# Optimization experiments

Hardware: AMD Instinct MI355X
Metric: run time of the kernel (lower is better)

Reference implementation:

```python
import jax, jax.numpy as jnp
import numpy as np

H = 64  # hidden size

def setup_inputs() -> dict:
    key = jax.random.key(0)
    ks = jax.random.split(key, 7)
    B, T = 256, 5000
    s = 1.0 / np.sqrt(H)  # PyTorch LSTM init scale
    return {
        "x":    jax.random.normal(ks[0], (B, T), dtype=jnp.float32),
        "W_ih": jax.random.uniform(ks[1], (4 * H, 1), jnp.float32, -s, s),
        "W_hh": jax.random.uniform(ks[2], (4 * H, H), jnp.float32, -s, s),
        "b_ih": jax.random.uniform(ks[3], (4 * H,), jnp.float32, -s, s),
        "b_hh": jax.random.uniform(ks[4], (4 * H,), jnp.float32, -s, s),
        "W_fc": jax.random.uniform(ks[5], (128, H), jnp.float32, -s, s),
        "b_fc": jax.random.uniform(ks[6], (128,), jnp.float32, -s, s),
    }

def _lstm_last_hidden(x, W_ih, W_hh, b_ih, b_hh):
    # x: [B, T]; returns last hidden state h_T: [B, H]
    B, T = x.shape
    # input projection for all timesteps at once: [B, T, 4H]
    # (input_size == 1, so this is an outer product with W_ih[:, 0])
    x_proj = x[:, :, None] * W_ih[:, 0][None, None, :] + (b_ih + b_hh)

    def step(carry, xp_t):
        h, c = carry
        gates = xp_t + h @ W_hh.T  # [B, 4H]
        i = jax.nn.sigmoid(gates[:, 0 * H:1 * H])
        f = jax.nn.sigmoid(gates[:, 1 * H:2 * H])
        g = jnp.tanh(gates[:, 2 * H:3 * H])
        o = jax.nn.sigmoid(gates[:, 3 * H:4 * H])
        c = f * c + i * g
        h = o * jnp.tanh(c)
        return (h, c), None

    h0 = jnp.zeros((B, H), x.dtype)
    c0 = jnp.zeros((B, H), x.dtype)
    (h, c), _ = jax.lax.scan(step, (h0, c0), jnp.swapaxes(x_proj, 0, 1))
    return h

def reference(x, W_ih, W_hh, b_ih, b_hh, W_fc, b_fc):
    h_last = _lstm_last_hidden(x, W_ih, W_hh, b_ih, b_hh)  # [B, H]
    return jax.nn.relu(h_last @ W_fc.T + b_fc)  # [B, 128]
```

## Files before the change

kernel.cpp:

```cpp
#include <hip/hip_runtime.h>


#define LSTM_H 64
#define LSTM_T 5000
#define LSTM_B 256

typedef float v2f __attribute__((ext_vector_type(2)));

__device__ __forceinline__ void pk_fma_acc(v2f& acc, v2f a, v2f b) {
    asm("v_pk_fma_f32 %0, %1, %2, %0" : "+v"(acc) : "v"(a), "v"(b));
}

__device__ __forceinline__ float fast_rcp(float v) {
    return __builtin_amdgcn_rcpf(v);
}

__global__ __launch_bounds__(256) void ECGLSTM_lstm_fused(
    const float* __restrict__ x,
    const float* __restrict__ W_ih,
    const float* __restrict__ W_hh,
    const float* __restrict__ b_ih,
    const float* __restrict__ b_hh,
    const float* __restrict__ W_fc,
    const float* __restrict__ b_fc,
    float* __restrict__ out)
{
    const int tid  = threadIdx.x;
    const int lane = tid & 63;
    const int b    = blockIdx.x;

    __shared__ float xch[LSTM_T];
    __shared__ float hbuf[2][LSTM_H];
    __shared__ float gbuf[2][4 * LSTM_H];

    const float* xb = x + b * LSTM_T;
    for (int i = tid; i < LSTM_T; i += 256) xch[i] = xb[i];

    v2f w[LSTM_H / 2];
    {
        const float4* wrow = reinterpret_cast<const float4*>(W_hh + tid * LSTM_H);
        #pragma unroll
        for (int i = 0; i < LSTM_H / 4; ++i) {
            float4 v = wrow[i];
            w[2 * i]     = v2f{v.x, v.y};
            w[2 * i + 1] = v2f{v.z, v.w};
        }
    }
    const float wih  = W_ih[tid];
    const float bias = b_ih[tid] + b_hh[tid];
    const bool  is_tanh = ((tid >> 6) == 2);

    float c = 0.0f;
    hbuf[0][lane] = 0.0f;
    __syncthreads();

    #define LSTM_STEP(t, P)                                                    \
    {                                                                          \
        const float xv = xch[(t)];                          \
        v2f A = {0.f, 0.f}, C = {0.f, 0.f};                                    \
        const float4* h4 = reinterpret_cast<const float4*>(hbuf[(P)]);         \
        _Pragma("unroll")                                                      \
        for (int i = 0; i < LSTM_H / 4; ++i) {                                 \
            float4 hv = h4[i];                             \
            pk_fma_acc(A, v2f{hv.x, hv.y}, w[2 * i]);                          \
            pk_fma_acc(C, v2f{hv.z, hv.w}, w[2 * i + 1]);                      \
        }                                                                      \
        float g = fmaf(xv, wih, bias) + ((A.x + A.y) + (C.x + C.y));           \
        float act;                                                             \
        if (is_tanh) {                                                         \
            float e = __expf(2.0f * g);                                        \
            act = 1.0f - 2.0f * fast_rcp(e + 1.0f);                            \
        } else {                                                               \
            float e = __expf(-g);                                              \
            act = fast_rcp(1.0f + e);                                          \
        }                                                                      \
        gbuf[(P)][tid] = act;                                                  \
        __syncthreads();                                  \
        const float ig = gbuf[(P)][lane];                                      \
        const float fg = gbuf[(P)][LSTM_H + lane];                             \
        const float gg = gbuf[(P)][2 * LSTM_H + lane];                         \
        const float og = gbuf[(P)][3 * LSTM_H + lane];                         \
        c = fmaf(fg, c, ig * gg);                                              \
        float e2 = __expf(2.0f * c);                                           \
        float th = 1.0f - 2.0f * fast_rcp(e2 + 1.0f);                          \
        hbuf[1 - (P)][lane] = og * th;                    \
    }

    for (int t = 0; t < LSTM_T; t += 2) {
        LSTM_STEP(t, 0);
        LSTM_STEP(t + 1, 1);
    }
    #undef LSTM_STEP

    if (tid < 128) {
        float s = b_fc[tid];
        const float4* wf = reinterpret_cast<const float4*>(W_fc + tid * LSTM_H);
        const float4* h4 = reinterpret_cast<const float4*>(hbuf[0]);
        #pragma unroll
        for (int i = 0; i < LSTM_H / 4; ++i) {
            float4 wv = wf[i];
            float4 hv = h4[i];
            s = fmaf(hv.x, wv.x, s);
            s = fmaf(hv.y, wv.y, s);
            s = fmaf(hv.z, wv.z, s);
            s = fmaf(hv.w, wv.w, s);
        }
        out[b * 128 + tid] = fmaxf(s, 0.0f);
    }
}

extern "C" void kernel_launch(void* const* d_in, const int* in_sizes, int n_in,
                              void* d_out, int out_size, void* d_ws, size_t ws_size,
                              hipStream_t stream) {
    const float* x    = (const float*)d_in[0];
    const float* W_ih = (const float*)d_in[1];
    const float* W_hh = (const float*)d_in[2];
    const float* b_ih = (const float*)d_in[3];
    const float* b_hh = (const float*)d_in[4];
    const float* W_fc = (const float*)d_in[5];
    const float* b_fc = (const float*)d_in[6];
    float* out = (float*)d_out;

    ECGLSTM_lstm_fused<<<LSTM_B, 256, 0, stream>>>(
        x, W_ih, W_hh, b_ih, b_hh, W_fc, b_fc, out);
}
```

Before: 2.075 ms.

## Restructure LSTM step to two waves with DPP/swizzle hidden-state broadcast

Each block now runs two wavefronts instead of four, and each thread computes two gate rows. The recurrent hidden vector no longer goes through shared memory. It is broadcast inside the wave with DPP row rotates, ds_swizzle and ds_bpermute, and the weight columns are pre-permuted to match that rotated order. Only the gate activations are still exchanged between the two waves through shared memory, which cuts barrier participants and LDS traffic on the serial critical path. In exchange each thread holds twice as many weight registers and does twice the FMAs per step, and the lane-rotation permutation logic is intricate.

```diff
diff --git a/kernel.cpp b/kernel.cpp
--- a/kernel.cpp
+++ b/kernel.cpp
@@ -10,12 +10,28 @@
 __device__ __forceinline__ void pk_fma_acc(v2f& acc, v2f a, v2f b) {
     asm("v_pk_fma_f32 %0, %1, %2, %0" : "+v"(acc) : "v"(a), "v"(b));
 }
-
 __device__ __forceinline__ float fast_rcp(float v) {
     return __builtin_amdgcn_rcpf(v);
 }
+template<int J>
+__device__ __forceinline__ float row_ror(float v) {
+    if constexpr (J == 0) return v;
+    else return __builtin_bit_cast(float,
+        __builtin_amdgcn_mov_dpp(__builtin_bit_cast(int, v),
+                                 0x120 + J, 0xF, 0xF, false));
+}
+__device__ __forceinline__ float swz16(float v) {
+    return __builtin_bit_cast(float,
+        __builtin_amdgcn_ds_swizzle(__builtin_bit_cast(int, v), 0x401F));
+}
+__device__ __forceinline__ float bperm(int addr, float v) {
+    return __builtin_bit_cast(float,
+        __builtin_amdgcn_ds_bpermute(addr, __builtin_bit_cast(int, v)));
+}
 
-__global__ __launch_bounds__(256) void ECGLSTM_lstm_fused(
+__global__ __attribute__((amdgpu_flat_work_group_size(128, 128),
+                          amdgpu_waves_per_eu(1, 1)))
+void ECGLSTM_lstm_2w(
     const float* __restrict__ x,
     const float* __restrict__ W_ih,
     const float* __restrict__ W_hh,
@@ -27,63 +43,89 @@
 {
     const int tid  = threadIdx.x;
     const int lane = tid & 63;
+    const bool w1  = (tid >> 6) != 0;
     const int b    = blockIdx.x;
 
     __shared__ float xch[LSTM_T];
-    __shared__ float hbuf[2][LSTM_H];
-    __shared__ float gbuf[2][4 * LSTM_H];
+    __shared__ float ex[2][4][LSTM_H];
+    __shared__ float hfin[LSTM_H];
 
     const float* xb = x + b * LSTM_T;
-    for (int i = tid; i < LSTM_T; i += 256) xch[i] = xb[i];
+    for (int i = tid; i < LSTM_T; i += 128) xch[i] = xb[i];
 
-    v2f w[LSTM_H / 2];
-    {
-        const float4* wrow = reinterpret_cast<const float4*>(W_hh + tid * LSTM_H);
-        #pragma unroll
-        for (int i = 0; i < LSTM_H / 4; ++i) {
-            float4 v = wrow[i];
-            w[2 * i]     = v2f{v.x, v.y};
-            w[2 * i + 1] = v2f{v.z, v.w};
-        }
+    int dirp = __builtin_amdgcn_mov_dpp(lane & 15, 0x121, 0xF, 0xF, false);
+    const int e = (__builtin_amdgcn_readlane(dirp, 0) == 1) ? 1 : -1;
+
+    const int GA = w1 ? 2 : 0;
+    const int GB = w1 ? 3 : 1;
+    const int rowA = GA * LSTM_H + lane;
+    const int rowB = GB * LSTM_H + lane;
+    v2f wa2[32], wb2[32];
+    #pragma unroll
+    for (int m2 = 0; m2 < 32; ++m2) {
+        const int m0 = 2 * m2, m1 = 2 * m2 + 1;
+        const int k0 = ((lane & 48) ^ ((m0 >> 4) << 4)) | ((lane + e * (m0 & 15)) & 15);
+        const int k1 = ((lane & 48) ^ ((m1 >> 4) << 4)) | ((lane + e * (m1 & 15)) & 15);
+        wa2[m2] = v2f{W_hh[rowA * LSTM_H + k0], W_hh[rowA * LSTM_H + k1]};
+        wb2[m2] = v2f{W_hh[rowB * LSTM_H + k0], W_hh[rowB * LSTM_H + k1]};
     }
-    const float wih  = W_ih[tid];
-    const float bias = b_ih[tid] + b_hh[tid];
-    const bool  is_tanh = ((tid >> 6) == 2);
+    const float wihA  = W_ih[rowA],  wihB  = W_ih[rowB];
+    const float biasA = b_ih[rowA] + b_hh[rowA];
+    const float biasB = b_ih[rowB] + b_hh[rowB];
+    const float aexpA = w1 ? -2.0f : -1.0f;
+    const float smulA = w1 ?  2.0f :  1.0f;
+    const float daddA = w1 ? -1.0f :  0.0f;
+    const int wsl = w1 ? 2 : 0;
+    const int osl = w1 ? 0 : 2;
+    const int a32 = (lane ^ 32) << 2, a48 = (lane ^ 48) << 2;
 
-    float c = 0.0f;
-    hbuf[0][lane] = 0.0f;
+    float h = 0.0f, c = 0.0f;
+    float b0 = 0.0f, b1 = 0.0f, b2 = 0.0f, b3 = 0.0f;
     __syncthreads();
+
+    #define DOT_CJ(cc, j2, bb)                                                 \
+    {                                                                          \
+        float h0 = row_ror<2*(j2)>(bb);                                        \
+        float h1 = row_ror<2*(j2)+1>(bb);                                      \
+        v2f h2{h0, h1};                                                        \
+        pk_fma_acc(aA[(cc)&1], h2, wa2[8*(cc)+(j2)]);                          \
+        pk_fma_acc(aB[(cc)&1], h2, wb2[8*(cc)+(j2)]);                          \
+    }
+    #define DOT_CHUNK(cc, bb) \
+        DOT_CJ(cc,0,bb) DOT_CJ(cc,1,bb) DOT_CJ(cc,2,bb) DOT_CJ(cc,3,bb) \
+        DOT_CJ(cc,4,bb) DOT_CJ(cc,5,bb) DOT_CJ(cc,6,bb) DOT_CJ(cc,7,bb)
 
     #define LSTM_STEP(t, P)                                                    \
     {                                                                          \
-        const float xv = xch[(t)];                          \
-        v2f A = {0.f, 0.f}, C = {0.f, 0.f};                                    \
-        const float4* h4 = reinterpret_cast<const float4*>(hbuf[(P)]);         \
-        _Pragma("unroll")                                                      \
-        for (int i = 0; i < LSTM_H / 4; ++i) {                                 \
-            float4 hv = h4[i];                             \
-            pk_fma_acc(A, v2f{hv.x, hv.y}, w[2 * i]);                          \
-            pk_fma_acc(C, v2f{hv.z, hv.w}, w[2 * i + 1]);                      \
-        }                                                                      \
-        float g = fmaf(xv, wih, bias) + ((A.x + A.y) + (C.x + C.y));           \
-        float act;                                                             \
-        if (is_tanh) {                                                         \
-            float e = __expf(2.0f * g);                                        \
-            act = 1.0f - 2.0f * fast_rcp(e + 1.0f);                            \
-        } else {                                                               \
-            float e = __expf(-g);                                              \
-            act = fast_rcp(1.0f + e);                                          \
-        }                                                                      \
-        gbuf[(P)][tid] = act;                                                  \
+        const float xv = xch[(t)];                                             \
+        v2f aA[2] = {v2f{0.f,0.f}, v2f{0.f,0.f}};                              \
+        v2f aB[2] = {v2f{0.f,0.f}, v2f{0.f,0.f}};                              \
+        DOT_CHUNK(0, b0) DOT_CHUNK(1, b1) DOT_CHUNK(2, b2) DOT_CHUNK(3, b3)    \
+        float dA = (aA[0].x + aA[0].y) + (aA[1].x + aA[1].y);                  \
+        float dB = (aB[0].x + aB[0].y) + (aB[1].x + aB[1].y);                  \
+        float gA = fmaf(xv, wihA, biasA) + dA;                                 \
+        float gB = fmaf(xv, wihB, biasB) + dB;                                 \
+        float eA = __expf(aexpA * gA);                                         \
+        float actA = fmaf(smulA, fast_rcp(1.0f + eA), daddA);                  \
+        float eB = __expf(-gB);                                                \
+        float actB = fast_rcp(1.0f + eB);                                      \
+        ex[(P)][wsl][lane]     = actA;                                         \
+        ex[(P)][wsl + 1][lane] = actB;                                         \
         __syncthreads();                                  \
-        const float ig = gbuf[(P)][lane];                                      \
-        const float fg = gbuf[(P)][LSTM_H + lane];                             \
-        const float gg = gbuf[(P)][2 * LSTM_H + lane];                         \
-        const float og = gbuf[(P)][3 * LSTM_H + lane];                         \
+        float o0 = ex[(P)][osl][lane];                                         \
+        float o1 = ex[(P)][osl + 1][lane];                                     \
+        float ig = w1 ? o0 : actA;                                             \
+        float fg = w1 ? o1 : actB;                                             \
+        float gg = w1 ? actA : o0;                                             \
+        float og = w1 ? actB : o1;                                             \
         c = fmaf(fg, c, ig * gg);                                              \
         float e2 = __expf(2.0f * c);                                           \
         float th = 1.0f - 2.0f * fast_rcp(e2 + 1.0f);                          \
-        hbuf[1 - (P)][lane] = og * th;                    \
+        h = og * th;                                                           \
+        b0 = h;                                                                \
+        b1 = swz16(h);                                                         \
+        b2 = bperm(a32, h);                                                    \
+        b3 = bperm(a48, h);                                                    \
     }
 
     for (int t = 0; t < LSTM_T; t += 2) {
@@ -91,11 +133,15 @@
         LSTM_STEP(t + 1, 1);
     }
     #undef LSTM_STEP
+    #undef DOT_CHUNK
+    #undef DOT_CJ
 
-    if (tid < 128) {
+    if (tid < LSTM_H) hfin[tid] = h;
+    __syncthreads();
+    {
         float s = b_fc[tid];
         const float4* wf = reinterpret_cast<const float4*>(W_fc + tid * LSTM_H);
-        const float4* h4 = reinterpret_cast<const float4*>(hbuf[0]);
+        const float4* h4 = reinterpret_cast<const float4*>(hfin);
         #pragma unroll
         for (int i = 0; i < LSTM_H / 4; ++i) {
             float4 wv = wf[i];
@@ -121,6 +167,6 @@
     const float* b_fc = (const float*)d_in[6];
     float* out = (float*)d_out;
 
-    ECGLSTM_lstm_fused<<<LSTM_B, 256, 0, stream>>>(
-        x, W_ih, W_hh, b_ih, b_hh, W_fc, b_fc, out);
+    hipLaunchKernelGGL(ECGLSTM_lstm_2w, dim3(LSTM_B), dim3(128), 0, stream,
+                       x, W_ih, W_hh, b_ih, b_hh, W_fc, b_fc, out);
 }
```

Result: slower. 2.196 ms (+5.9%).
